# Performance work log

Measured on AMD Instinct MI355X. Metric: run time of the kernel, lower is better.

The kernel has to match this reference:

```python
import jax, jax.numpy as jnp
import numpy as np

B, T, D, H, C = 128, 1024, 512, 512, 2


def setup_inputs() -> dict:
    key = jax.random.key(0)
    ks = jax.random.split(key, 4)
    return {
        "x": jax.random.normal(ks[0], (B, T, D), dtype=jnp.float32),
        "W": jax.random.normal(ks[1], (D, 3 * H), dtype=jnp.float32) * 0.02,
        "R": jax.random.normal(ks[2], (H, 3 * H), dtype=jnp.float32) * 0.02,
        "b_i": jnp.zeros((3 * H,), jnp.float32),
        "b_r": jnp.zeros((3 * H,), jnp.float32),
        "Wf": jax.random.normal(ks[3], (H, C), dtype=jnp.float32) * 0.02,
        "bf": jnp.zeros((C,), jnp.float32),
    }


def _gru_last(x, W, R, b_i, b_r):
    # Keras GRU v2 (reset_after=True), gate order [z, r, h]; eval mode (no dropout).
    b, t, d = x.shape
    h_dim = R.shape[0]
    # Input projection for all timesteps in one big GEMM: [B,T,3H]
    xp = jnp.einsum('btd,dk->btk', x, W) + b_i
    xp = jnp.moveaxis(xp, 1, 0)  # time-major [T,B,3H]

    def step(h, xt):
        hp = h @ R + b_r                      # [B,3H]
        xz, xr, xh = jnp.split(xt, 3, axis=-1)
        hz, hr, hhp = jnp.split(hp, 3, axis=-1)
        z = jax.nn.sigmoid(xz + hz)
        r = jax.nn.sigmoid(xr + hr)
        hh = jnp.tanh(xh + r * hhp)
        h_new = z * h + (1.0 - z) * hh
        return h_new, None

    h0 = jnp.zeros((b, h_dim), x.dtype)
    h_last, _ = jax.lax.scan(step, h0, xp)
    return h_last  # [B,H] (return_sequences=False)


def reference(x, W, R, b_i, b_r, Wf, bf):
    h = _gru_last(x, W, R, b_i, b_r)
    return h @ Wf + bf  # logits [B, num_classes]
```

## Files before the change

kernel.cpp:

```cpp
#include <hip/hip_runtime.h>
#include <stdint.h>


#define NWG   256
#define WB    8
#define BT    192
#define Tseq  1024
#define Bdim  128
#define Ddim  512
#define Hdim  512
#define NH3   1536

typedef __attribute__((ext_vector_type(8))) short short8;
typedef __attribute__((ext_vector_type(4))) float f32x4;

union U4S8 { uint4 u; short8 s; };

__device__ __forceinline__ unsigned short f2bf(float f) {
  unsigned u = __float_as_uint(f);
  unsigned r = (u + 0x7FFFu + ((u >> 16) & 1u)) >> 16;
  return (unsigned short)r;
}
__device__ __forceinline__ unsigned pack2(float a, float b) {
  return (unsigned)f2bf(a) | ((unsigned)f2bf(b) << 16);
}
__device__ __forceinline__ float bsig(float x) { return 1.f / (1.f + __expf(-x)); }
__device__ __forceinline__ float btanh(float x) {
  float a = fabsf(x);
  float e = __expf(-2.f * a);
  float t = (1.f - e) / (1.f + e);
  return x < 0.f ? -t : t;
}

__device__ __forceinline__ void stage16x512(unsigned short* lds, const float* src,
                                            size_t rowStride, int tid) {
  for (int c = tid; c < 1024; c += BT) {
    int row = c >> 6, cb = c & 63;
    const float* p = src + (size_t)row * rowStride + (size_t)cb * 8;
    float4 a = *(const float4*)p;
    float4 b = *(const float4*)(p + 4);
    uint4 v;
    v.x = pack2(a.x, a.y); v.y = pack2(a.z, a.w);
    v.z = pack2(b.x, b.y); v.w = pack2(b.z, b.w);
    int byte = (row << 10) | (((cb << 4) ^ ((row & 7) << 4)));
    *(uint4*)((char*)lds + byte) = v;
  }
}

__device__ __forceinline__ short8 readA(const unsigned short* lds, int lane, int kk) {
  int row = lane & 15, kg = lane >> 4;
  int byte = (row << 10) | ((((kk << 6) + (kg << 4)) ^ ((row & 7) << 4)));
  U4S8 t;
  t.u = *(const uint4*)((const char*)lds + byte);
  return t.s;
}

__global__ __launch_bounds__(BT) void gru_persist(
    const float* __restrict__ x, const float* __restrict__ W,
    const float* __restrict__ R, const float* __restrict__ b_i,
    const float* __restrict__ b_r, int* __restrict__ cnt,
    float* __restrict__ h0, float* __restrict__ h1) {
  __shared__ alignas(16) unsigned short hA[16 * 512];
  __shared__ alignas(16) unsigned short xA[16 * 512];
  __shared__ float tg[4][256];

  const int tid  = threadIdx.x;
  const int lane = tid & 63;
  const int g    = tid >> 6;
  const int wb   = blockIdx.x & (WB - 1);
  const int wj   = blockIdx.x >> 3;
  const int brow0 = wb << 4;
  const int col0  = wj << 4;
  const int colL  = lane & 15;
  const int kg    = lane >> 4;
  const int gc    = g * Hdim + col0 + colL;

  short8 Wf_[16], Rf_[16];
#pragma unroll
  for (int kk = 0; kk < 16; ++kk) {
    short8 w, r;
#pragma unroll
    for (int j = 0; j < 8; ++j) {
      int k = kk * 32 + kg * 8 + j;
      w[j] = (short)f2bf(W[(size_t)k * NH3 + gc]);
      r[j] = (short)f2bf(R[(size_t)k * NH3 + gc]);
    }
    Wf_[kk] = w; Rf_[kk] = r;
  }
  const float bi = b_i[gc];
  const float br = b_r[gc];

  stage16x512(xA, x + (size_t)brow0 * (Tseq * Ddim), (size_t)Tseq * Ddim, tid);
  __syncthreads();
  f32x4 accX = {0.f, 0.f, 0.f, 0.f};
#pragma unroll
  for (int kk = 0; kk < 16; ++kk)
    accX = __builtin_amdgcn_mfma_f32_16x16x32_bf16(readA(xA, lane, kk), Wf_[kk], accX, 0, 0, 0);

  for (int t = 0; t < Tseq; ++t) {
    const float* hin  = (t & 1) ? h1 : h0;
    float*       hout = (t & 1) ? h0 : h1;

    stage16x512(hA, hin + (size_t)brow0 * Hdim, (size_t)Hdim, tid);
    __syncthreads();

    f32x4 accH = {0.f, 0.f, 0.f, 0.f};
#pragma unroll
    for (int kk = 0; kk < 16; ++kk)
      accH = __builtin_amdgcn_mfma_f32_16x16x32_bf16(readA(hA, lane, kk), Rf_[kk], accH, 0, 0, 0);

#pragma unroll
    for (int r4 = 0; r4 < 4; ++r4) {
      int e = ((kg * 4 + r4) << 4) | colL;
      if (g == 0)      tg[0][e] = accX[r4] + accH[r4] + bi + br;
      else if (g == 1) tg[1][e] = accX[r4] + accH[r4] + bi + br;
      else {           tg[2][e] = accX[r4] + bi;
                       tg[3][e] = accH[r4] + br; }
    }
    __syncthreads();

    for (int e2 = tid; e2 < 128; e2 += BT) {
      int row = e2 >> 3;
      int col = (e2 & 7) << 1;
      int ez  = (row << 4) | col;
      float z0 = bsig(tg[0][ez]),     z1 = bsig(tg[0][ez + 1]);
      float r0 = bsig(tg[1][ez]),     r1 = bsig(tg[1][ez + 1]);
      float hh0 = btanh(tg[2][ez]     + r0 * tg[3][ez]);
      float hh1 = btanh(tg[2][ez + 1] + r1 * tg[3][ez + 1]);
      size_t idx = (size_t)(brow0 + row) * Hdim + col0 + col;
      float ho0 = hin[idx], ho1 = hin[idx + 1];
      union { float f[2]; unsigned long long u; } pk;
      pk.f[0] = z0 * ho0 + (1.f - z0) * hh0;
      pk.f[1] = z1 * ho1 + (1.f - z1) * hh1;
      __hip_atomic_store((unsigned long long*)&hout[idx], pk.u,
                         __ATOMIC_RELAXED, __HIP_MEMORY_SCOPE_AGENT);
    }
    __syncthreads();

    if (tid == 0)
      __hip_atomic_fetch_add(&cnt[t], 1, __ATOMIC_RELAXED, __HIP_MEMORY_SCOPE_AGENT);

    int tt = (t + 1 < Tseq) ? t + 1 : Tseq - 1;
    stage16x512(xA, x + (size_t)brow0 * (Tseq * Ddim) + (size_t)tt * Ddim,
                (size_t)Tseq * Ddim, tid);
    __syncthreads();
    accX = (f32x4){0.f, 0.f, 0.f, 0.f};
#pragma unroll
    for (int kk = 0; kk < 16; ++kk)
      accX = __builtin_amdgcn_mfma_f32_16x16x32_bf16(readA(xA, lane, kk), Wf_[kk], accX, 0, 0, 0);

    if (tid == 0) {
      while (__hip_atomic_load(&cnt[t], __ATOMIC_RELAXED, __HIP_MEMORY_SCOPE_AGENT) < NWG) {}
      __builtin_amdgcn_fence(__ATOMIC_ACQUIRE, "agent");
    }
    __syncthreads();
  }
}

__global__ __launch_bounds__(64) void logits_kernel(const float* __restrict__ hbuf,
                                                    const float* __restrict__ Wf,
                                                    const float* __restrict__ bf,
                                                    float* __restrict__ out) {
  int b = blockIdx.x, l = threadIdx.x;
  const float* hr = hbuf + (size_t)b * Hdim;
  float c0 = 0.f, c1 = 0.f;
#pragma unroll
  for (int i = 0; i < 8; ++i) {
    int k = l * 8 + i;
    float h = hr[k];
    c0 += h * Wf[k * 2 + 0];
    c1 += h * Wf[k * 2 + 1];
  }
  for (int off = 32; off > 0; off >>= 1) {
    c0 += __shfl_down(c0, off);
    c1 += __shfl_down(c1, off);
  }
  if (l == 0) {
    out[b * 2 + 0] = c0 + bf[0];
    out[b * 2 + 1] = c1 + bf[1];
  }
}

extern "C" void kernel_launch(void* const* d_in, const int* in_sizes, int n_in,
                              void* d_out, int out_size, void* d_ws, size_t ws_size,
                              hipStream_t stream) {
  (void)in_sizes; (void)n_in; (void)out_size; (void)ws_size;
  const float* x   = (const float*)d_in[0];
  const float* W   = (const float*)d_in[1];
  const float* R   = (const float*)d_in[2];
  const float* b_i = (const float*)d_in[3];
  const float* b_r = (const float*)d_in[4];
  const float* Wf  = (const float*)d_in[5];
  const float* bf  = (const float*)d_in[6];

  char* ws = (char*)d_ws;
  int*   cnt = (int*)ws;
  float* h0  = (float*)(ws + 4096);
  float* h1  = (float*)(ws + 4096 + Bdim * Hdim * 4);

  hipMemsetAsync(ws, 0, 4096 + Bdim * Hdim * 4, stream);

  hipLaunchKernelGGL(gru_persist, dim3(NWG), dim3(BT), 0, stream,
                     x, W, R, b_i, b_r, cnt, h0, h1);
  hipLaunchKernelGGL(logits_kernel, dim3(Bdim), dim3(64), 0, stream,
                     h0, Wf, bf, (float*)d_out);
}
```

Before: 8.774 ms.

## Halve persistent workgroups, replace counter barrier with per-WG progress flags

Moves the persistent GRU kernel from 256 workgroups of 3 waves to 128 workgroups of 6 waves, so each workgroup computes 32 hidden columns and fewer participants join each timestep's grid barrier. The per-timestep atomic counter is replaced by per-workgroup progress flags that one wave polls with 64-bit loads and a wave vote, with an explicit release fence before publishing. The hidden-state staging now uses agent-scope atomic loads, and the MFMA chains are split into two accumulators for more instruction-level parallelism. The cost is more work per workgroup on the serial path, and correctness now rests on the new fence and flag protocol.

Measured after the change: 12.27 ms. 39.8% more time.

```diff
diff --git a/kernel.cpp b/kernel.cpp
--- a/kernel.cpp
+++ b/kernel.cpp
@@ -2,9 +2,8 @@
 #include <stdint.h>
 
 
-#define NWG   256
-#define WB    8
-#define BT    192
+#define NWG   128
+#define BT    384
 #define Tseq  1024
 #define Bdim  128
 #define Ddim  512
@@ -15,6 +14,7 @@
 typedef __attribute__((ext_vector_type(4))) float f32x4;
 
 union U4S8 { uint4 u; short8 s; };
+union PK8 { float f[2]; unsigned long long u; };
 
 __device__ __forceinline__ unsigned short f2bf(float f) {
   unsigned u = __float_as_uint(f);
@@ -32,11 +32,11 @@
   return x < 0.f ? -t : t;
 }
 
-__device__ __forceinline__ void stage16x512(unsigned short* lds, const float* src,
-                                            size_t rowStride, int tid) {
+__device__ __forceinline__ void stageX(unsigned short* lds, const float* src,
+                                       int tid) {
   for (int c = tid; c < 1024; c += BT) {
     int row = c >> 6, cb = c & 63;
-    const float* p = src + (size_t)row * rowStride + (size_t)cb * 8;
+    const float* p = src + (size_t)row * ((size_t)Tseq * Ddim) + (size_t)cb * 8;
     float4 a = *(const float4*)p;
     float4 b = *(const float4*)(p + 4);
     uint4 v;
@@ -47,6 +47,20 @@
   }
 }
 
+__device__ __forceinline__ void stageH(unsigned short* lds, const float* src,
+                                       int brow0, int tid) {
+  for (int c = tid; c < 4096; c += BT) {
+    int row = c >> 8, cp = c & 255;
+    const long long* p =
+        (const long long*)(src + (size_t)(brow0 + row) * Hdim + (size_t)cp * 2);
+    long long raw = __hip_atomic_load(p, __ATOMIC_RELAXED, __HIP_MEMORY_SCOPE_AGENT);
+    PK8 pk; pk.u = (unsigned long long)raw;
+    unsigned w = pack2(pk.f[0], pk.f[1]);
+    int byte = (row << 10) | (((cp << 2) ^ ((row & 7) << 4)));
+    *(unsigned*)((char*)lds + byte) = w;
+  }
+}
+
 __device__ __forceinline__ short8 readA(const unsigned short* lds, int lane, int kk) {
   int row = lane & 15, kg = lane >> 4;
   int byte = (row << 10) | ((((kk << 6) + (kg << 4)) ^ ((row & 7) << 4)));
@@ -55,103 +69,121 @@
   return t.s;
 }
 
-__global__ __launch_bounds__(BT) void gru_persist(
+__global__ __launch_bounds__(BT, 2) void gru_persist(
     const float* __restrict__ x, const float* __restrict__ W,
     const float* __restrict__ R, const float* __restrict__ b_i,
-    const float* __restrict__ b_r, int* __restrict__ cnt,
+    const float* __restrict__ b_r, int* __restrict__ prog,
     float* __restrict__ h0, float* __restrict__ h1) {
   __shared__ alignas(16) unsigned short hA[16 * 512];
   __shared__ alignas(16) unsigned short xA[16 * 512];
-  __shared__ float tg[4][256];
+  __shared__ float tg[4][512];
 
   const int tid  = threadIdx.x;
   const int lane = tid & 63;
-  const int g    = tid >> 6;
-  const int wb   = blockIdx.x & (WB - 1);
-  const int wj   = blockIdx.x >> 3;
-  const int brow0 = wb << 4;
-  const int col0  = wj << 4;
+  const int w    = tid >> 6;
+  const int g    = w >> 1;
+  const int c    = w & 1;
+  const int wg   = blockIdx.x;
+  const int brow0 = (wg & 7) << 4;
+  const int cg    = wg >> 3;
   const int colL  = lane & 15;
   const int kg    = lane >> 4;
-  const int gc    = g * Hdim + col0 + colL;
+  const int gcol  = cg * 32 + c * 16 + colL;
+  const int gc    = g * Hdim + gcol;
 
   short8 Wf_[16], Rf_[16];
 #pragma unroll
   for (int kk = 0; kk < 16; ++kk) {
-    short8 w, r;
+    short8 wv, rv;
 #pragma unroll
     for (int j = 0; j < 8; ++j) {
       int k = kk * 32 + kg * 8 + j;
-      w[j] = (short)f2bf(W[(size_t)k * NH3 + gc]);
-      r[j] = (short)f2bf(R[(size_t)k * NH3 + gc]);
-    }
-    Wf_[kk] = w; Rf_[kk] = r;
+      wv[j] = (short)f2bf(W[(size_t)k * NH3 + gc]);
+      rv[j] = (short)f2bf(R[(size_t)k * NH3 + gc]);
+    }
+    Wf_[kk] = wv; Rf_[kk] = rv;
   }
   const float bi = b_i[gc];
   const float br = b_r[gc];
 
-  stage16x512(xA, x + (size_t)brow0 * (Tseq * Ddim), (size_t)Tseq * Ddim, tid);
+  stageX(xA, x + (size_t)brow0 * (Tseq * Ddim), tid);
   __syncthreads();
-  f32x4 accX = {0.f, 0.f, 0.f, 0.f};
-#pragma unroll
-  for (int kk = 0; kk < 16; ++kk)
-    accX = __builtin_amdgcn_mfma_f32_16x16x32_bf16(readA(xA, lane, kk), Wf_[kk], accX, 0, 0, 0);
+  f32x4 aX0 = {0,0,0,0}, aX1 = {0,0,0,0};
+#pragma unroll
+  for (int kk = 0; kk < 8; ++kk) {
+    aX0 = __builtin_amdgcn_mfma_f32_16x16x32_bf16(readA(xA, lane, 2*kk),   Wf_[2*kk],   aX0, 0, 0, 0);
+    aX1 = __builtin_amdgcn_mfma_f32_16x16x32_bf16(readA(xA, lane, 2*kk+1), Wf_[2*kk+1], aX1, 0, 0, 0);
+  }
 
   for (int t = 0; t < Tseq; ++t) {
     const float* hin  = (t & 1) ? h1 : h0;
     float*       hout = (t & 1) ? h0 : h1;
 
-    stage16x512(hA, hin + (size_t)brow0 * Hdim, (size_t)Hdim, tid);
-    __syncthreads();
-
-    f32x4 accH = {0.f, 0.f, 0.f, 0.f};
-#pragma unroll
-    for (int kk = 0; kk < 16; ++kk)
-      accH = __builtin_amdgcn_mfma_f32_16x16x32_bf16(readA(hA, lane, kk), Rf_[kk], accH, 0, 0, 0);
+    stageH(hA, hin, brow0, tid);
+    __syncthreads();
+
+    f32x4 aH0 = {0,0,0,0}, aH1 = {0,0,0,0};
+#pragma unroll
+    for (int kk = 0; kk < 8; ++kk) {
+      aH0 = __builtin_amdgcn_mfma_f32_16x16x32_bf16(readA(hA, lane, 2*kk),   Rf_[2*kk],   aH0, 0, 0, 0);
+      aH1 = __builtin_amdgcn_mfma_f32_16x16x32_bf16(readA(hA, lane, 2*kk+1), Rf_[2*kk+1], aH1, 0, 0, 0);
+    }
 
 #pragma unroll
     for (int r4 = 0; r4 < 4; ++r4) {
-      int e = ((kg * 4 + r4) << 4) | colL;
-      if (g == 0)      tg[0][e] = accX[r4] + accH[r4] + bi + br;
-      else if (g == 1) tg[1][e] = accX[r4] + accH[r4] + bi + br;
-      else {           tg[2][e] = accX[r4] + bi;
-                       tg[3][e] = accH[r4] + br; }
-    }
-    __syncthreads();
-
-    for (int e2 = tid; e2 < 128; e2 += BT) {
-      int row = e2 >> 3;
-      int col = (e2 & 7) << 1;
-      int ez  = (row << 4) | col;
+      int row = kg * 4 + r4;
+      int e = row * 32 + c * 16 + colL;
+      float vx = aX0[r4] + aX1[r4];
+      float vh = aH0[r4] + aH1[r4];
+      if (g == 0)      tg[0][e] = vx + vh + bi + br;
+      else if (g == 1) tg[1][e] = vx + vh + bi + br;
+      else {           tg[2][e] = vx + bi;
+                       tg[3][e] = vh + br; }
+    }
+    __syncthreads();
+
+    for (int e2 = tid; e2 < 256; e2 += BT) {
+      int row = e2 >> 4;
+      int col = (e2 & 15) << 1;
+      int ez  = row * 32 + col;
       float z0 = bsig(tg[0][ez]),     z1 = bsig(tg[0][ez + 1]);
       float r0 = bsig(tg[1][ez]),     r1 = bsig(tg[1][ez + 1]);
       float hh0 = btanh(tg[2][ez]     + r0 * tg[3][ez]);
       float hh1 = btanh(tg[2][ez + 1] + r1 * tg[3][ez + 1]);
-      size_t idx = (size_t)(brow0 + row) * Hdim + col0 + col;
-      float ho0 = hin[idx], ho1 = hin[idx + 1];
-      union { float f[2]; unsigned long long u; } pk;
-      pk.f[0] = z0 * ho0 + (1.f - z0) * hh0;
-      pk.f[1] = z1 * ho1 + (1.f - z1) * hh1;
+      size_t idx = (size_t)(brow0 + row) * Hdim + cg * 32 + col;
+      long long raw = __hip_atomic_load((const long long*)&hin[idx],
+                                        __ATOMIC_RELAXED, __HIP_MEMORY_SCOPE_AGENT);
+      PK8 po; po.u = (unsigned long long)raw;
+      PK8 pk;
+      pk.f[0] = z0 * po.f[0] + (1.f - z0) * hh0;
+      pk.f[1] = z1 * po.f[1] + (1.f - z1) * hh1;
       __hip_atomic_store((unsigned long long*)&hout[idx], pk.u,
                          __ATOMIC_RELAXED, __HIP_MEMORY_SCOPE_AGENT);
     }
+    __builtin_amdgcn_fence(__ATOMIC_RELEASE, "agent");
     __syncthreads();
 
     if (tid == 0)
-      __hip_atomic_fetch_add(&cnt[t], 1, __ATOMIC_RELAXED, __HIP_MEMORY_SCOPE_AGENT);
+      __hip_atomic_store(&prog[wg], t + 1, __ATOMIC_RELAXED, __HIP_MEMORY_SCOPE_AGENT);
 
     int tt = (t + 1 < Tseq) ? t + 1 : Tseq - 1;
-    stage16x512(xA, x + (size_t)brow0 * (Tseq * Ddim) + (size_t)tt * Ddim,
-                (size_t)Tseq * Ddim, tid);
-    __syncthreads();
-    accX = (f32x4){0.f, 0.f, 0.f, 0.f};
-#pragma unroll
-    for (int kk = 0; kk < 16; ++kk)
-      accX = __builtin_amdgcn_mfma_f32_16x16x32_bf16(readA(xA, lane, kk), Wf_[kk], accX, 0, 0, 0);
-
-    if (tid == 0) {
-      while (__hip_atomic_load(&cnt[t], __ATOMIC_RELAXED, __HIP_MEMORY_SCOPE_AGENT) < NWG) {}
-      __builtin_amdgcn_fence(__ATOMIC_ACQUIRE, "agent");
+    stageX(xA, x + (size_t)brow0 * (Tseq * Ddim) + (size_t)tt * Ddim, tid);
+    __syncthreads();
+    aX0 = (f32x4){0,0,0,0}; aX1 = (f32x4){0,0,0,0};
+#pragma unroll
+    for (int kk = 0; kk < 8; ++kk) {
+      aX0 = __builtin_amdgcn_mfma_f32_16x16x32_bf16(readA(xA, lane, 2*kk),   Wf_[2*kk],   aX0, 0, 0, 0);
+      aX1 = __builtin_amdgcn_mfma_f32_16x16x32_bf16(readA(xA, lane, 2*kk+1), Wf_[2*kk+1], aX1, 0, 0, 0);
+    }
+
+    if (w == 0) {
+      const long long* pp = (const long long*)&prog[lane * 2];
+      int need = t + 1;
+      while (true) {
+        long long v = __hip_atomic_load(pp, __ATOMIC_RELAXED, __HIP_MEMORY_SCOPE_AGENT);
+        int a = (int)v, b = (int)(v >> 32);
+        if (__all(a >= need && b >= need)) break;
+      }
     }
     __syncthreads();
   }
@@ -194,14 +226,14 @@
   const float* bf  = (const float*)d_in[6];
 
   char* ws = (char*)d_ws;
-  int*   cnt = (int*)ws;
-  float* h0  = (float*)(ws + 4096);
-  float* h1  = (float*)(ws + 4096 + Bdim * Hdim * 4);
+  int*   prog = (int*)ws;
+  float* h0   = (float*)(ws + 4096);
+  float* h1   = (float*)(ws + 4096 + Bdim * Hdim * 4);
 
   hipMemsetAsync(ws, 0, 4096 + Bdim * Hdim * 4, stream);
 
   hipLaunchKernelGGL(gru_persist, dim3(NWG), dim3(BT), 0, stream,
-                     x, W, R, b_i, b_r, cnt, h0, h1);
+                     x, W, R, b_i, b_r, prog, h0, h1);
   hipLaunchKernelGGL(logits_kernel, dim3(Bdim), dim3(64), 0, stream,
                      h0, Wf, bf, (float*)d_out);
 }
```
